# Kernel tuning notes

Measured on AMD Instinct MI355X. Metric: run time of the kernel, lower is better.

## Reference

```python
import jax, jax.numpy as jnp
import numpy as np

EPS = 1e-5

def _ln(x, w, b):
    m = jnp.mean(x, -1, keepdims=True)
    v = jnp.mean((x - m) ** 2, -1, keepdims=True)
    return (x - m) * jax.lax.rsqrt(v + EPS) * w + b

def _silu(x):
    return x * jax.nn.sigmoid(x)

def _mamba(x, in_proj_w, conv_w, conv_b, x_proj_w, dt_proj_w, dt_proj_b, A_log, D, out_proj_w):
    # x: [Bc, L, d_model]; standard mamba_ssm Mamba block math
    Bc, L, _ = x.shape
    d_inner = conv_b.shape[0]
    d_state = A_log.shape[1]
    dt_rank = dt_proj_w.shape[0]
    xz = x @ in_proj_w                          # [Bc, L, 2*d_inner]
    xm, z = jnp.split(xz, 2, axis=-1)
    # causal depthwise conv1d (pad left d_conv-1, truncate to L)
    xm_t = jnp.transpose(xm, (0, 2, 1))         # [Bc, d_inner, L]
    xm_t = jax.lax.conv_general_dilated(
        xm_t, conv_w[:, None, :], (1,), [(conv_w.shape[-1] - 1, 0)],
        dimension_numbers=('NCH', 'OIH', 'NCH'), feature_group_count=d_inner)
    xm = _silu(jnp.transpose(xm_t, (0, 2, 1)) + conv_b)   # [Bc, L, d_inner]
    x_dbl = xm @ x_proj_w                        # [Bc, L, dt_rank + 2*d_state]
    dt_r = x_dbl[..., :dt_rank]
    Bm = x_dbl[..., dt_rank:dt_rank + d_state]
    Cm = x_dbl[..., dt_rank + d_state:]
    dt = jax.nn.softplus(dt_r @ dt_proj_w + dt_proj_b)    # [Bc, L, d_inner]
    A = -jnp.exp(A_log)                          # [d_inner, d_state]

    def step(h, inp):
        xt, dtt, Bt, Ct = inp                    # [Bc,d_inner],[Bc,d_inner],[Bc,d_state],[Bc,d_state]
        dA = jnp.exp(dtt[:, :, None] * A)
        h = dA * h + (dtt * xt)[:, :, None] * Bt[:, None, :]
        y = jnp.einsum('bds,bs->bd', h, Ct)
        return h, y

    h0 = jnp.zeros((Bc, d_inner, d_state), x.dtype)
    xs = (jnp.transpose(xm, (1, 0, 2)), jnp.transpose(dt, (1, 0, 2)),
          jnp.transpose(Bm, (1, 0, 2)), jnp.transpose(Cm, (1, 0, 2)))
    _, ys = jax.lax.scan(step, h0, xs)
    y = jnp.transpose(ys, (1, 0, 2)) + xm * D    # [Bc, L, d_inner]
    y = y * _silu(z)
    return y @ out_proj_w                        # [Bc, L, d_model]

def _pvmamba(x, ln_w, ln_b, skip_scale, proj_w, proj_b, mp):
    # x: [B, H, W, C]; 4 channel-chunks share one Mamba -> batch them as lanes
    B, H, W, C = x.shape
    n = H * W
    d = C // 4
    xf = x.reshape(B, n, C)
    xn = _ln(xf, ln_w, ln_b)
    xc = jnp.transpose(xn.reshape(B, n, 4, d), (2, 0, 1, 3)).reshape(4 * B, n, d)
    ym = _mamba(xc, *mp) + skip_scale * xc
    ym = jnp.transpose(ym.reshape(4, B, n, d), (1, 2, 0, 3)).reshape(B, n, C)
    ym = _ln(ym, ln_w, ln_b)                     # second LN reuses same params (as in source)
    out = ym @ proj_w + proj_b
    return out.reshape(B, H, W, -1)

def _down(x, w):
    # Conv2d k=2 s=2 no bias, exact non-overlapping patch contraction; w: [O, I, 2, 2]
    B, H, W, C = x.shape
    xr = jnp.transpose(x, (0, 3, 1, 2)).reshape(B, C, H // 2, 2, W // 2, 2)
    y = jnp.einsum('bcipjq,ocpq->boij', xr, w)
    return jnp.transpose(y, (0, 2, 3, 1))

def _up(x, w):
    # ConvTranspose2d k=2 s=2 no bias; w: [I, O, 2, 2] (torch layout)
    B, H, W, C = x.shape
    xc = jnp.transpose(x, (0, 3, 1, 2))
    y = jnp.einsum('bcij,copq->boipjq', xc, w).reshape(B, w.shape[1], 2 * H, 2 * W)
    return jnp.transpose(y, (0, 2, 3, 1))

def _mpma(x, ln_w, ln_b, skip_scale, proj_w, proj_b, in_proj_w, conv_w, conv_b,
          x_proj_w, dt_proj_w, dt_proj_b, A_log, D, out_proj_w, down_w, up_w):
    mp = (in_proj_w, conv_w, conv_b, x_proj_w, dt_proj_w, dt_proj_b, A_log, D, out_proj_w)
    xh = jnp.transpose(x, (0, 2, 3, 1))          # NCHW -> NHWC
    outs = [_pvmamba(xh, ln_w, ln_b, skip_scale, proj_w, proj_b, mp)]
    xin = xh
    for _ in range(1, 5):
        xin = _down(xin, down_w)
        outs.append(_pvmamba(xin, ln_w, ln_b, skip_scale, proj_w, proj_b, mp))
    res = outs[-1]
    for l, od in enumerate(outs[-2::-1]):
        res = od + (1.0 / (l + 1)) * _up(res, up_w)
    return jnp.transpose(res, (0, 3, 2, 1))      # note: (0,3,2,1) as in source -> [B,C,W,H]

def setup_inputs() -> dict:
    B, C, HW = 8, 64, 128
    d_model, d_inner, d_state, d_conv, dt_rank = 16, 32, 16, 4, 1
    key = jax.random.key(0)
    ks = jax.random.split(key, 10)
    x = jax.random.normal(ks[0], (B, C, HW, HW), jnp.float32)
    return {
        'x': x,
        'ln_w': jnp.ones((C,), jnp.float32),
        'ln_b': jnp.zeros((C,), jnp.float32),
        'skip_scale': jnp.ones((1,), jnp.float32),
        'proj_w': jax.random.normal(ks[1], (C, C), jnp.float32) * 0.05,
        'proj_b': jnp.zeros((C,), jnp.float32),
        'in_proj_w': jax.random.normal(ks[2], (d_model, 2 * d_inner), jnp.float32) * 0.1,
        'conv_w': jax.random.normal(ks[3], (d_inner, d_conv), jnp.float32) * 0.2,
        'conv_b': jnp.zeros((d_inner,), jnp.float32),
        'x_proj_w': jax.random.normal(ks[4], (d_inner, dt_rank + 2 * d_state), jnp.float32) * 0.1,
        'dt_proj_w': jax.random.normal(ks[5], (dt_rank, d_inner), jnp.float32) * 0.5,
        'dt_proj_b': jnp.full((d_inner,), -4.0, jnp.float32),
        'A_log': jnp.broadcast_to(jnp.log(jnp.arange(1, d_state + 1, dtype=jnp.float32)), (d_inner, d_state)),
        'D': jnp.ones((d_inner,), jnp.float32),
        'out_proj_w': jax.random.normal(ks[6], (d_inner, d_model), jnp.float32) * 0.1,
        'down_w': jax.random.normal(ks[7], (C, C, 2, 2), jnp.float32) * 0.05,
        'up_w': jax.random.normal(ks[8], (C, C, 2, 2), jnp.float32) * 0.05,
    }

def reference(x, ln_w, ln_b, skip_scale, proj_w, proj_b, in_proj_w, conv_w, conv_b,
              x_proj_w, dt_proj_w, dt_proj_b, A_log, D, out_proj_w, down_w, up_w):
    return _mpma(x, ln_w, ln_b, skip_scale, proj_w, proj_b, in_proj_w, conv_w, conv_b,
                 x_proj_w, dt_proj_w, dt_proj_b, A_log, D, out_proj_w, down_w, up_w)
```

## Files before the change

kernel.cpp:

```cpp
#include <hip/hip_runtime.h>

#define TMAX 128

__device__ __forceinline__ float silu_f(float x) {
    return x / (1.f + __expf(-x));
}
__device__ __forceinline__ float softplus_f(float x) {
    return (x > 20.f) ? x : log1pf(__expf(x));
}

__global__ __launch_bounds__(256) void k_tr_in(const float* __restrict__ x, float* __restrict__ xh) {
    __shared__ float tile[128 * 65];
    int h = blockIdx.x, b = blockIdx.y;
    const float* ip = x + (size_t)b * 64 * 16384 + (size_t)h * 128;
    for (int i = threadIdx.x; i < 64 * 128; i += 256) {
        int c = i >> 7, w = i & 127;
        tile[w * 65 + c] = ip[(size_t)c * 16384 + w];
    }
    __syncthreads();
    float* op = xh + ((size_t)(b * 128 + h)) * 128 * 64;
    for (int i = threadIdx.x; i < 128 * 64; i += 256) {
        int w = i >> 6, c = i & 63;
        op[i] = tile[w * 65 + c];
    }
}

__global__ __launch_bounds__(256) void k_tr_out(const float* __restrict__ res, float* __restrict__ out) {
    __shared__ float tile[64 * 129];
    int w = blockIdx.x, b = blockIdx.y;
    const float* ip = res + (size_t)b * 16384 * 64 + (size_t)w * 64;
    for (int i = threadIdx.x; i < 128 * 64; i += 256) {
        int h = i >> 6, c = i & 63;
        tile[c * 129 + h] = ip[(size_t)h * 128 * 64 + c];
    }
    __syncthreads();
    float* op = out + (size_t)b * 64 * 16384 + (size_t)w * 128;
    for (int i = threadIdx.x; i < 64 * 128; i += 256) {
        int c = i >> 7, hh = i & 127;
        op[(size_t)c * 16384 + hh] = tile[c * 129 + hh];
    }
}

__global__ __launch_bounds__(256) void k_down(const float* __restrict__ in, float* __restrict__ out,
                                              const float* __restrict__ dwp, int Ho, int Wo, int ntot) {
    __shared__ float dw[16384];
    for (int i = threadIdx.x; i < 16384; i += 256) {
        int o = i & 63, cpq = i >> 6;
        dw[cpq * 64 + o] = dwp[o * 256 + cpq];
    }
    __syncthreads();
    int gid = blockIdx.x * 256 + threadIdx.x;
    if (gid >= ntot) return;
    int og = gid & 3, pix = gid >> 2;
    int j = pix % Wo, i2 = (pix / Wo) % Ho, b = pix / (Wo * Ho);
    const float* ip = in + (((size_t)b * (2 * Ho) + 2 * i2) * (size_t)(2 * Wo) + 2 * j) * 64;
    float acc[16];
#pragma unroll
    for (int m = 0; m < 16; ++m) acc[m] = 0.f;
    for (int p = 0; p < 2; ++p) {
        for (int q = 0; q < 2; ++q) {
            const float* xp = ip + ((size_t)p * (2 * Wo) + q) * 64;
            for (int c = 0; c < 64; ++c) {
                float xv = xp[c];
                const float* wrow = &dw[(c * 4 + p * 2 + q) * 64 + og * 16];
#pragma unroll
                for (int m = 0; m < 16; ++m) acc[m] = fmaf(xv, wrow[m], acc[m]);
            }
        }
    }
    float* op = out + (size_t)pix * 64 + og * 16;
#pragma unroll
    for (int m = 0; m < 4; ++m) {
        float4 v = make_float4(acc[m * 4], acc[m * 4 + 1], acc[m * 4 + 2], acc[m * 4 + 3]);
        *(float4*)(op + m * 4) = v;
    }
}

__global__ __launch_bounds__(256) void k_up(const float* __restrict__ src, float* __restrict__ dst,
                                            const float* __restrict__ uwp, int H, int W, float coef, int ntot) {
    __shared__ float uw[16384];
    for (int i = threadIdx.x; i < 16384; i += 256) {
        int o = i & 63, cpq = i >> 6;
        int c = cpq >> 2, pq = cpq & 3;
        uw[cpq * 64 + o] = uwp[c * 256 + o * 4 + pq];
    }
    __syncthreads();
    int gid = blockIdx.x * 256 + threadIdx.x;
    if (gid >= ntot) return;
    int og = gid & 3, pix = gid >> 2;
    int x = pix % W, y = (pix / W) % H, b = pix / (W * H);
    int Hs = H >> 1, Ws = W >> 1;
    int pq = (y & 1) * 2 + (x & 1);
    const float* sp = src + (((size_t)b * Hs + (y >> 1)) * (size_t)Ws + (x >> 1)) * 64;
    float acc[16];
#pragma unroll
    for (int m = 0; m < 16; ++m) acc[m] = 0.f;
    for (int c = 0; c < 64; ++c) {
        float xv = sp[c];
        const float* wrow = &uw[(c * 4 + pq) * 64 + og * 16];
#pragma unroll
        for (int m = 0; m < 16; ++m) acc[m] = fmaf(xv, wrow[m], acc[m]);
    }
    float* op = dst + (size_t)pix * 64 + og * 16;
#pragma unroll
    for (int m = 0; m < 4; ++m) {
        float4 cur = *(float4*)(op + m * 4);
        cur.x += coef * acc[m * 4];
        cur.y += coef * acc[m * 4 + 1];
        cur.z += coef * acc[m * 4 + 2];
        cur.w += coef * acc[m * 4 + 3];
        *(float4*)(op + m * 4) = cur;
    }
}

__global__ __launch_bounds__(256) void k_ln(const float* __restrict__ in, float* __restrict__ out,
                                            const float* __restrict__ w, const float* __restrict__ bb, int ntok) {
    int t = blockIdx.x * 256 + threadIdx.x;
    if (t >= ntok) return;
    const float4* p = (const float4*)(in + (size_t)t * 64);
    float4 v[16];
    float s = 0.f;
#pragma unroll
    for (int i = 0; i < 16; ++i) {
        v[i] = p[i];
        s += v[i].x + v[i].y + v[i].z + v[i].w;
    }
    float m = s * (1.f / 64.f);
    float q = 0.f;
#pragma unroll
    for (int i = 0; i < 16; ++i) {
        float a = v[i].x - m, b2 = v[i].y - m, c = v[i].z - m, d = v[i].w - m;
        q += a * a + b2 * b2 + c * c + d * d;
    }
    float r = rsqrtf(q * (1.f / 64.f) + 1e-5f);
    float4* o = (float4*)(out + (size_t)t * 64);
    const float4* w4 = (const float4*)w;
    const float4* b4 = (const float4*)bb;
#pragma unroll
    for (int i = 0; i < 16; ++i) {
        float4 ww = w4[i], bbv = b4[i];
        float4 ov;
        ov.x = (v[i].x - m) * r * ww.x + bbv.x;
        ov.y = (v[i].y - m) * r * ww.y + bbv.y;
        ov.z = (v[i].z - m) * r * ww.z + bbv.z;
        ov.w = (v[i].w - m) * r * ww.w + bbv.w;
        o[i] = ov;
    }
}

__global__ __launch_bounds__(256) void k_post(const float* __restrict__ ym, float* __restrict__ outl,
                                              const float* __restrict__ lnw, const float* __restrict__ lnb,
                                              const float* __restrict__ proj_w, const float* __restrict__ proj_b,
                                              int ntok) {
    __shared__ float pw[4096];
    __shared__ float pb[64];
    __shared__ float lw[64], lb[64];
    for (int i = threadIdx.x; i < 4096; i += 256) pw[i] = proj_w[i];
    if (threadIdx.x < 64) {
        pb[threadIdx.x] = proj_b[threadIdx.x];
        lw[threadIdx.x] = lnw[threadIdx.x];
        lb[threadIdx.x] = lnb[threadIdx.x];
    }
    __syncthreads();
    int t = blockIdx.x * 256 + threadIdx.x;
    if (t >= ntok) return;
    const float4* p = (const float4*)(ym + (size_t)t * 64);
    float4 v[16];
    float s = 0.f;
#pragma unroll
    for (int i = 0; i < 16; ++i) {
        v[i] = p[i];
        s += v[i].x + v[i].y + v[i].z + v[i].w;
    }
    float m = s * (1.f / 64.f);
    float q = 0.f;
#pragma unroll
    for (int i = 0; i < 16; ++i) {
        float a = v[i].x - m, b2 = v[i].y - m, c = v[i].z - m, d = v[i].w - m;
        q += a * a + b2 * b2 + c * c + d * d;
    }
    float r = rsqrtf(q * (1.f / 64.f) + 1e-5f);
    float* op = outl + (size_t)t * 64;
    for (int half = 0; half < 2; ++half) {
        float acc[32];
#pragma unroll
        for (int o = 0; o < 32; ++o) acc[o] = pb[half * 32 + o];
#pragma unroll
        for (int i = 0; i < 16; ++i) {
            float vals[4] = {v[i].x, v[i].y, v[i].z, v[i].w};
#pragma unroll
            for (int k = 0; k < 4; ++k) {
                int c = i * 4 + k;
                float vn = (vals[k] - m) * r * lw[c] + lb[c];
                const float* wrow = &pw[c * 64 + half * 32];
#pragma unroll
                for (int o = 0; o < 32; ++o) acc[o] = fmaf(vn, wrow[o], acc[o]);
            }
        }
#pragma unroll
        for (int mq = 0; mq < 8; ++mq) {
            float4 ov = make_float4(acc[mq * 4], acc[mq * 4 + 1], acc[mq * 4 + 2], acc[mq * 4 + 3]);
            *(float4*)(op + half * 32 + mq * 4) = ov;
        }
    }
}

template <int PHASE>
__global__ __launch_bounds__(256, 2) void k_scan(const float* __restrict__ xn,
                                                 float* __restrict__ Pbuf, float* __restrict__ Hbuf,
                                                 const float* __restrict__ hinbuf, float* __restrict__ ym,
                                                 const float* __restrict__ in_proj_w, const float* __restrict__ conv_w,
                                                 const float* __restrict__ conv_b, const float* __restrict__ x_proj_w,
                                                 const float* __restrict__ dt_w, const float* __restrict__ dt_b,
                                                 const float* __restrict__ A_log, const float* __restrict__ Dvec,
                                                 const float* __restrict__ out_proj_w, const float* __restrict__ skip_scale,
                                                 int n, int nch) {
    __shared__ float Wm[16][32];
    __shared__ float Wz[16][32];
    __shared__ float cw[32][4];
    __shared__ float cb[32];
    __shared__ float Wxp[32][33];
    __shared__ float dtw[32], dtb[32];
    __shared__ float Ash[32][16];
    __shared__ float Dsh[32];
    __shared__ float Wout[32][16];
    __shared__ float xmpre_y[(TMAX + 3) * 32];
    __shared__ float dt_s[TMAX][32];
    __shared__ float xm_s[TMAX][32];
    __shared__ float Bs[TMAX][16];
    __shared__ float Cs[TMAX][16];

    const int tid = threadIdx.x;
    const int chunk = blockIdx.x;
    const int seq = blockIdx.y;
    const int g = seq >> 3, b = seq & 7;
    const int t0 = chunk * TMAX;
    const int Tc = (n - t0 < TMAX) ? (n - t0) : TMAX;

    for (int i = tid; i < 16 * 32; i += 256) {
        int k = i >> 5, d = i & 31;
        Wm[k][d] = in_proj_w[k * 64 + d];
        Wz[k][d] = in_proj_w[k * 64 + 32 + d];
    }
    for (int i = tid; i < 32 * 4; i += 256) cw[i >> 2][i & 3] = conv_w[i];
    if (tid < 32) {
        cb[tid] = conv_b[tid];
        dtw[tid] = dt_w[tid];
        dtb[tid] = dt_b[tid];
        Dsh[tid] = Dvec[tid];
    }
    for (int i = tid; i < 32 * 33; i += 256) Wxp[i / 33][i % 33] = x_proj_w[i];
    for (int i = tid; i < 32 * 16; i += 256) {
        Ash[i >> 4][i & 15] = -__expf(A_log[i]);
        Wout[i >> 4][i & 15] = out_proj_w[i];
    }
    __syncthreads();

    const float* xbase = xn + (size_t)b * n * 64 + g * 16;

    if (tid < Tc + 3) {
        int t = t0 + tid - 3;
        float* dst = &xmpre_y[tid * 32];
        if (t < 0) {
#pragma unroll
            for (int d = 0; d < 32; ++d) dst[d] = 0.f;
        } else {
            const float4* xp = (const float4*)(xbase + (size_t)t * 64);
            float4 x0 = xp[0], x1 = xp[1], x2 = xp[2], x3 = xp[3];
            float xc[16] = {x0.x, x0.y, x0.z, x0.w, x1.x, x1.y, x1.z, x1.w,
                            x2.x, x2.y, x2.z, x2.w, x3.x, x3.y, x3.z, x3.w};
#pragma unroll
            for (int d = 0; d < 32; ++d) {
                float a = 0.f;
#pragma unroll
                for (int k = 0; k < 16; ++k) a = fmaf(xc[k], Wm[k][d], a);
                dst[d] = a;
            }
        }
    }
    __syncthreads();

    if (tid < Tc) {
        float xmv[32];
#pragma unroll
        for (int d = 0; d < 32; ++d) {
            float a = cb[d];
#pragma unroll
            for (int k = 0; k < 4; ++k) a = fmaf(xmpre_y[(tid + k) * 32 + d], cw[d][k], a);
            float sv = silu_f(a);
            xmv[d] = sv;
            xm_s[tid][d] = sv;
        }
        float dtr = 0.f;
#pragma unroll
        for (int d = 0; d < 32; ++d) dtr = fmaf(xmv[d], Wxp[d][0], dtr);
#pragma unroll
        for (int s = 0; s < 16; ++s) {
            float bv = 0.f;
#pragma unroll
            for (int d = 0; d < 32; ++d) bv = fmaf(xmv[d], Wxp[d][1 + s], bv);
            Bs[tid][s] = bv;
            if (PHASE == 1) {
                float cv = 0.f;
#pragma unroll
                for (int d = 0; d < 32; ++d) cv = fmaf(xmv[d], Wxp[d][17 + s], cv);
                Cs[tid][s] = cv;
            }
        }
#pragma unroll
        for (int d = 0; d < 32; ++d) dt_s[tid][d] = softplus_f(fmaf(dtr, dtw[d], dtb[d]));
    }
    __syncthreads();

    const int d = tid >> 3;
    const int s0 = (tid & 7) * 2;
    const float a0 = Ash[d][s0], a1 = Ash[d][s0 + 1];
    float h0, h1;
    const size_t cbi = ((size_t)seq * nch + chunk) * 512 + tid * 2;
    if (PHASE == 1) {
        float2 hi = *(const float2*)&hinbuf[cbi];
        h0 = hi.x;
        h1 = hi.y;
    } else {
        h0 = 0.f;
        h1 = 0.f;
    }
    float sdt = 0.f;
#pragma unroll 2
    for (int t = 0; t < Tc; ++t) {
        float dtv = dt_s[t][d];
        float u = dtv * xm_s[t][d];
        float2 bb2 = *(const float2*)&Bs[t][s0];
        float e0 = __expf(dtv * a0), e1 = __expf(dtv * a1);
        h0 = fmaf(e0, h0, u * bb2.x);
        h1 = fmaf(e1, h1, u * bb2.y);
        if (PHASE == 0) {
            sdt += dtv;
        } else {
            float2 cc = *(const float2*)&Cs[t][s0];
            float pp = fmaf(h0, cc.x, h1 * cc.y);
            pp += __shfl_xor(pp, 1);
            pp += __shfl_xor(pp, 2);
            pp += __shfl_xor(pp, 4);
            if ((tid & 7) == 0) xmpre_y[t * 32 + d] = pp;
        }
    }
    if (PHASE == 0) {
        float2 pv;
        pv.x = __expf(a0 * sdt);
        pv.y = __expf(a1 * sdt);
        *(float2*)&Pbuf[cbi] = pv;
        float2 hv;
        hv.x = h0;
        hv.y = h1;
        *(float2*)&Hbuf[cbi] = hv;
    } else {
        __syncthreads();
        if (tid < Tc) {
            int t = t0 + tid;
            const float4* xp = (const float4*)(xbase + (size_t)t * 64);
            float4 x0 = xp[0], x1 = xp[1], x2 = xp[2], x3 = xp[3];
            float xc[16] = {x0.x, x0.y, x0.z, x0.w, x1.x, x1.y, x1.z, x1.w,
                            x2.x, x2.y, x2.z, x2.w, x3.x, x3.y, x3.z, x3.w};
            float yv[32];
#pragma unroll
            for (int dd = 0; dd < 32; ++dd) {
                float zz = 0.f;
#pragma unroll
                for (int k = 0; k < 16; ++k) zz = fmaf(xc[k], Wz[k][dd], zz);
                float yb = xmpre_y[tid * 32 + dd] + xm_s[tid][dd] * Dsh[dd];
                yv[dd] = yb * silu_f(zz);
            }
            float ss = skip_scale[0];
            float* ymtok = ym + ((size_t)b * n + t) * 64 + g * 16;
#pragma unroll
            for (int jq = 0; jq < 4; ++jq) {
                float4 ov;
                float o0 = 0.f, o1 = 0.f, o2 = 0.f, o3 = 0.f;
#pragma unroll
                for (int dd = 0; dd < 32; ++dd) {
                    o0 = fmaf(yv[dd], Wout[dd][jq * 4 + 0], o0);
                    o1 = fmaf(yv[dd], Wout[dd][jq * 4 + 1], o1);
                    o2 = fmaf(yv[dd], Wout[dd][jq * 4 + 2], o2);
                    o3 = fmaf(yv[dd], Wout[dd][jq * 4 + 3], o3);
                }
                ov.x = o0 + ss * xc[jq * 4 + 0];
                ov.y = o1 + ss * xc[jq * 4 + 1];
                ov.z = o2 + ss * xc[jq * 4 + 2];
                ov.w = o3 + ss * xc[jq * 4 + 3];
                *(float4*)(ymtok + jq * 4) = ov;
            }
        }
    }
}

__global__ __launch_bounds__(256) void k_scanB(const float* __restrict__ P, const float* __restrict__ Hl,
                                               float* __restrict__ hin, int nch) {
    int idx = blockIdx.x * 256 + threadIdx.x;
    int seq = idx >> 9, ds = idx & 511;
    size_t base = (size_t)seq * nch * 512 + ds;
    float h = 0.f;
    for (int k = 0; k < nch; ++k) {
        hin[base + (size_t)k * 512] = h;
        h = fmaf(P[base + (size_t)k * 512], h, Hl[base + (size_t)k * 512]);
    }
}

extern "C" void kernel_launch(void* const* d_in, const int* in_sizes, int n_in,
                              void* d_out, int out_size, void* d_ws, size_t ws_size,
                              hipStream_t stream) {
    (void)in_sizes; (void)n_in; (void)out_size; (void)ws_size;
    const float* x          = (const float*)d_in[0];
    const float* ln_w       = (const float*)d_in[1];
    const float* ln_b       = (const float*)d_in[2];
    const float* skip_scale = (const float*)d_in[3];
    const float* proj_w     = (const float*)d_in[4];
    const float* proj_b     = (const float*)d_in[5];
    const float* in_proj_w  = (const float*)d_in[6];
    const float* conv_w     = (const float*)d_in[7];
    const float* conv_b     = (const float*)d_in[8];
    const float* x_proj_w   = (const float*)d_in[9];
    const float* dt_proj_w  = (const float*)d_in[10];
    const float* dt_proj_b  = (const float*)d_in[11];
    const float* A_log      = (const float*)d_in[12];
    const float* Dv         = (const float*)d_in[13];
    const float* out_proj_w = (const float*)d_in[14];
    const float* down_w     = (const float*)d_in[15];
    const float* up_w       = (const float*)d_in[16];
    float* out = (float*)d_out;
    float* ws = (float*)d_ws;

    static const int nl[5] = {16384, 4096, 1024, 256, 64};
    static const size_t off_xh[5] = {0, 8388608, 10485760, 11010048, 11141120};
    static const size_t off_out[5] = {11173888, 19562496, 21659648, 22183936, 22315008};
    const size_t off_xn = 22347776;
    const size_t off_P = 30736384;
    const size_t off_H = 32833536;
    const size_t off_hin = 34930688;
    const size_t off_ym = 0;

    k_tr_in<<<dim3(128, 8), dim3(256), 0, stream>>>(x, ws + off_xh[0]);

    for (int l = 0; l < 4; ++l) {
        int Ho = 128 >> (l + 1);
        int ntot = 8 * Ho * Ho * 4;
        k_down<<<dim3((ntot + 255) / 256), dim3(256), 0, stream>>>(ws + off_xh[l], ws + off_xh[l + 1],
                                                                   down_w, Ho, Ho, ntot);
    }

    for (int l = 0; l < 5; ++l) {
        int n = nl[l];
        int ntok = 8 * n;
        int nch = (n + TMAX - 1) / TMAX;
        k_ln<<<dim3((ntok + 255) / 256), dim3(256), 0, stream>>>(ws + off_xh[l], ws + off_xn, ln_w, ln_b, ntok);
        k_scan<0><<<dim3(nch, 32), dim3(256), 0, stream>>>(ws + off_xn, ws + off_P, ws + off_H, nullptr, nullptr,
                                                           in_proj_w, conv_w, conv_b, x_proj_w, dt_proj_w, dt_proj_b,
                                                           A_log, Dv, out_proj_w, skip_scale, n, nch);
        k_scanB<<<dim3(64), dim3(256), 0, stream>>>(ws + off_P, ws + off_H, ws + off_hin, nch);
        k_scan<1><<<dim3(nch, 32), dim3(256), 0, stream>>>(ws + off_xn, nullptr, nullptr, ws + off_hin, ws + off_ym,
                                                           in_proj_w, conv_w, conv_b, x_proj_w, dt_proj_w, dt_proj_b,
                                                           A_log, Dv, out_proj_w, skip_scale, n, nch);
        k_post<<<dim3((ntok + 255) / 256), dim3(256), 0, stream>>>(ws + off_ym, ws + off_out[l], ln_w, ln_b,
                                                                   proj_w, proj_b, ntok);
    }

    static const float coefs[4] = {1.f, 0.5f, 1.f / 3.f, 0.25f};
    for (int k = 0; k < 4; ++k) {
        int l = 3 - k;
        int H = 128 >> l;
        int ntot = 8 * H * H * 4;
        k_up<<<dim3((ntot + 255) / 256), dim3(256), 0, stream>>>(ws + off_out[l + 1], ws + off_out[l],
                                                                 up_w, H, H, coefs[k], ntot);
    }

    k_tr_out<<<dim3(128, 8), dim3(256), 0, stream>>>(ws + off_out[0], out);
}
```

Before: 1.636 ms.

## Precompute scan inputs once into fp16 stream; split chunked scan into pre/A/B/C kernels

LayerNorm, in_proj, conv, x_proj and dt projection now run once in a k_pre kernel. It writes dt, x, B and C as half2 into a time-contiguous stream buffer, replacing the old two-phase scan that recomputed these projections in both phases. The scan kernels then read compact fp16 data directly from global memory, and the final phase fuses LN recomputation, gating and out_proj. The trade-offs are fp16 rounding of scan inputs, per-step global loads with no shared staging, and extra launches when the workspace forces the sequences to be split.

```diff
diff --git a/kernel.cpp b/kernel.cpp
--- a/kernel.cpp
+++ b/kernel.cpp
@@ -1,4 +1,5 @@
 #include <hip/hip_runtime.h>
+#include <hip/hip_fp16.h>
 
 #define TMAX 128
 
@@ -113,38 +114,256 @@
     }
 }
 
-__global__ __launch_bounds__(256) void k_ln(const float* __restrict__ in, float* __restrict__ out,
-                                            const float* __restrict__ w, const float* __restrict__ bb, int ntok) {
-    int t = blockIdx.x * 256 + threadIdx.x;
-    if (t >= ntok) return;
-    const float4* p = (const float4*)(in + (size_t)t * 64);
-    float4 v[16];
-    float s = 0.f;
-#pragma unroll
-    for (int i = 0; i < 16; ++i) {
-        v[i] = p[i];
-        s += v[i].x + v[i].y + v[i].z + v[i].w;
-    }
-    float m = s * (1.f / 64.f);
-    float q = 0.f;
-#pragma unroll
-    for (int i = 0; i < 16; ++i) {
-        float a = v[i].x - m, b2 = v[i].y - m, c = v[i].z - m, d = v[i].w - m;
-        q += a * a + b2 * b2 + c * c + d * d;
-    }
-    float r = rsqrtf(q * (1.f / 64.f) + 1e-5f);
-    float4* o = (float4*)(out + (size_t)t * 64);
-    const float4* w4 = (const float4*)w;
-    const float4* b4 = (const float4*)bb;
-#pragma unroll
-    for (int i = 0; i < 16; ++i) {
-        float4 ww = w4[i], bbv = b4[i];
-        float4 ov;
-        ov.x = (v[i].x - m) * r * ww.x + bbv.x;
-        ov.y = (v[i].y - m) * r * ww.y + bbv.y;
-        ov.z = (v[i].z - m) * r * ww.z + bbv.z;
-        ov.w = (v[i].w - m) * r * ww.w + bbv.w;
-        o[i] = ov;
+__global__ __launch_bounds__(256) void k_pre(const float* __restrict__ xh, __half2* __restrict__ stream,
+                                             const float* __restrict__ lnw, const float* __restrict__ lnb,
+                                             const float* __restrict__ in_proj_w, const float* __restrict__ conv_w,
+                                             const float* __restrict__ conv_b, const float* __restrict__ x_proj_w,
+                                             const float* __restrict__ dt_w, const float* __restrict__ dt_b,
+                                             int n, int nseq, int seq_base) {
+    __shared__ float pre[259][33];
+    __shared__ float Wm[16][32];
+    __shared__ float Wxp[32][33];
+    __shared__ float cw[32][4];
+    __shared__ float cb[32], dtw[32], dtb[32];
+    __shared__ float lw[64], lb[64];
+    const int tid = threadIdx.x;
+    const int t0 = blockIdx.x * 256;
+    const int seqL = blockIdx.y;
+    const int seqG = seq_base + seqL;
+    const int b = seqG >> 2, g = seqG & 3;
+
+    for (int i = tid; i < 512; i += 256) Wm[i >> 5][i & 31] = in_proj_w[(i >> 5) * 64 + (i & 31)];
+    for (int i = tid; i < 32 * 33; i += 256) Wxp[i / 33][i % 33] = x_proj_w[i];
+    for (int i = tid; i < 128; i += 256) cw[i >> 2][i & 3] = conv_w[i];
+    if (tid < 32) { cb[tid] = conv_b[tid]; dtw[tid] = dt_w[tid]; dtb[tid] = dt_b[tid]; }
+    if (tid < 64) { lw[tid] = lnw[tid]; lb[tid] = lnb[tid]; }
+    __syncthreads();
+
+    const int Tcb = min(256, n - t0);
+    const int rows = Tcb + 3;
+    for (int r = tid; r < rows; r += 256) {
+        int t = t0 + r - 3;
+        if (t < 0) {
+#pragma unroll
+            for (int d = 0; d < 32; ++d) pre[r][d] = 0.f;
+        } else {
+            const float4* xp = (const float4*)(xh + ((size_t)b * n + t) * 64);
+            float4 v[16];
+            float s = 0.f;
+#pragma unroll
+            for (int i = 0; i < 16; ++i) { v[i] = xp[i]; s += v[i].x + v[i].y + v[i].z + v[i].w; }
+            float m = s * (1.f / 64.f);
+            float q = 0.f;
+#pragma unroll
+            for (int i = 0; i < 16; ++i) {
+                float a = v[i].x - m, b2 = v[i].y - m, c = v[i].z - m, dd = v[i].w - m;
+                q += a * a + b2 * b2 + c * c + dd * dd;
+            }
+            float rr = rsqrtf(q * (1.f / 64.f) + 1e-5f);
+            const float4* xg = (const float4*)(xh + ((size_t)b * n + t) * 64 + g * 16);
+            float xn16[16];
+#pragma unroll
+            for (int i = 0; i < 4; ++i) {
+                float4 u4 = xg[i];
+                int c0 = g * 16 + i * 4;
+                xn16[i * 4 + 0] = (u4.x - m) * rr * lw[c0 + 0] + lb[c0 + 0];
+                xn16[i * 4 + 1] = (u4.y - m) * rr * lw[c0 + 1] + lb[c0 + 1];
+                xn16[i * 4 + 2] = (u4.z - m) * rr * lw[c0 + 2] + lb[c0 + 2];
+                xn16[i * 4 + 3] = (u4.w - m) * rr * lw[c0 + 3] + lb[c0 + 3];
+            }
+#pragma unroll
+            for (int d = 0; d < 32; ++d) {
+                float a = 0.f;
+#pragma unroll
+                for (int j = 0; j < 16; ++j) a = fmaf(xn16[j], Wm[j][d], a);
+                pre[r][d] = a;
+            }
+        }
+    }
+    __syncthreads();
+
+    if (tid < Tcb) {
+        const int t = t0 + tid;
+        float xmv[32];
+#pragma unroll
+        for (int d = 0; d < 32; ++d) {
+            float a = cb[d];
+#pragma unroll
+            for (int k = 0; k < 4; ++k) a = fmaf(pre[tid + k][d], cw[d][k], a);
+            xmv[d] = silu_f(a);
+        }
+        float dtr = 0.f;
+#pragma unroll
+        for (int d = 0; d < 32; ++d) dtr = fmaf(xmv[d], Wxp[d][0], dtr);
+        const size_t sb = (size_t)seqL * n + t;
+#pragma unroll
+        for (int d = 0; d < 32; ++d) {
+            float dtv = softplus_f(fmaf(dtr, dtw[d], dtb[d]));
+            stream[(size_t)d * nseq * n + sb] = __floats2half2_rn(dtv, xmv[d]);
+        }
+#pragma unroll
+        for (int p = 0; p < 8; ++p) {
+            float b0 = 0.f, b1 = 0.f;
+#pragma unroll
+            for (int d = 0; d < 32; ++d) {
+                b0 = fmaf(xmv[d], Wxp[d][1 + 2 * p], b0);
+                b1 = fmaf(xmv[d], Wxp[d][2 + 2 * p], b1);
+            }
+            stream[(size_t)(32 + p) * nseq * n + sb] = __floats2half2_rn(b0, b1);
+        }
+#pragma unroll
+        for (int p = 0; p < 8; ++p) {
+            float c0 = 0.f, c1 = 0.f;
+#pragma unroll
+            for (int d = 0; d < 32; ++d) {
+                c0 = fmaf(xmv[d], Wxp[d][17 + 2 * p], c0);
+                c1 = fmaf(xmv[d], Wxp[d][18 + 2 * p], c1);
+            }
+            stream[(size_t)(40 + p) * nseq * n + sb] = __floats2half2_rn(c0, c1);
+        }
+    }
+}
+
+__global__ __launch_bounds__(256) void k_scanA(const __half2* __restrict__ stream, float* __restrict__ P,
+                                               float* __restrict__ H, const float* __restrict__ A_log,
+                                               int n, int nseq, int nch) {
+    const int tid = threadIdx.x;
+    const int d = tid >> 3, ss = tid & 7;
+    const int chunk = blockIdx.x, seqL = blockIdx.y;
+    const int t0 = chunk * TMAX;
+    const int Tc = min(TMAX, n - t0);
+    const float a0 = -__expf(A_log[d * 16 + 2 * ss]);
+    const float a1 = -__expf(A_log[d * 16 + 2 * ss + 1]);
+    const __half2* pdx = stream + ((size_t)d * nseq + seqL) * n + t0;
+    const __half2* pB = stream + ((size_t)(32 + ss) * nseq + seqL) * n + t0;
+    float h0 = 0.f, h1 = 0.f, sdt = 0.f;
+    for (int t = 0; t < Tc; ++t) {
+        float2 dx = __half22float2(pdx[t]);
+        float2 bv = __half22float2(pB[t]);
+        float u = dx.x * dx.y;
+        h0 = fmaf(__expf(a0 * dx.x), h0, u * bv.x);
+        h1 = fmaf(__expf(a1 * dx.x), h1, u * bv.y);
+        sdt += dx.x;
+    }
+    const size_t cbi = ((size_t)seqL * nch + chunk) * 512 + tid * 2;
+    *(float2*)&P[cbi] = make_float2(__expf(a0 * sdt), __expf(a1 * sdt));
+    *(float2*)&H[cbi] = make_float2(h0, h1);
+}
+
+__global__ __launch_bounds__(256) void k_scanB(const float* __restrict__ P, const float* __restrict__ Hl,
+                                               float* __restrict__ hin, int nch, int nseq) {
+    int idx = blockIdx.x * 256 + threadIdx.x;
+    if (idx >= nseq * 512) return;
+    int seq = idx >> 9, ds = idx & 511;
+    size_t base = (size_t)seq * nch * 512 + ds;
+    float h = 0.f;
+    for (int k = 0; k < nch; ++k) {
+        hin[base + (size_t)k * 512] = h;
+        h = fmaf(P[base + (size_t)k * 512], h, Hl[base + (size_t)k * 512]);
+    }
+}
+
+__global__ __launch_bounds__(256) void k_scanC(const __half2* __restrict__ stream, const float* __restrict__ hin,
+                                               const float* __restrict__ xh, float* __restrict__ ym,
+                                               const float* __restrict__ A_log,
+                                               const float* __restrict__ lnw, const float* __restrict__ lnb,
+                                               const float* __restrict__ in_proj_w, const float* __restrict__ Dvec,
+                                               const float* __restrict__ out_proj_w,
+                                               const float* __restrict__ skip_scale,
+                                               int n, int nseq, int seq_base, int nch) {
+    __shared__ float yb[TMAX][33];
+    __shared__ float Wz[16][32];
+    __shared__ float Wout[32][16];
+    __shared__ float lw[64], lb[64];
+    __shared__ float Dsh[32];
+    const int tid = threadIdx.x;
+    const int d = tid >> 3, ss = tid & 7;
+    const int chunk = blockIdx.x, seqL = blockIdx.y;
+    const int seqG = seq_base + seqL;
+    const int b = seqG >> 2, g = seqG & 3;
+    const int t0 = chunk * TMAX;
+    const int Tc = min(TMAX, n - t0);
+
+    for (int i = tid; i < 512; i += 256) Wz[i >> 5][i & 31] = in_proj_w[(i >> 5) * 64 + 32 + (i & 31)];
+    for (int i = tid; i < 512; i += 256) Wout[i >> 4][i & 15] = out_proj_w[i];
+    if (tid < 64) { lw[tid] = lnw[tid]; lb[tid] = lnb[tid]; }
+    if (tid < 32) Dsh[tid] = Dvec[tid];
+
+    const float a0 = -__expf(A_log[d * 16 + 2 * ss]);
+    const float a1 = -__expf(A_log[d * 16 + 2 * ss + 1]);
+    const __half2* pdx = stream + ((size_t)d * nseq + seqL) * n + t0;
+    const __half2* pB = stream + ((size_t)(32 + ss) * nseq + seqL) * n + t0;
+    const __half2* pC = stream + ((size_t)(40 + ss) * nseq + seqL) * n + t0;
+    const size_t cbi = ((size_t)seqL * nch + chunk) * 512 + tid * 2;
+    float2 hi2 = *(const float2*)&hin[cbi];
+    float h0 = hi2.x, h1 = hi2.y;
+
+    for (int t = 0; t < Tc; ++t) {
+        float2 dx = __half22float2(pdx[t]);
+        float2 bv = __half22float2(pB[t]);
+        float2 cv = __half22float2(pC[t]);
+        float u = dx.x * dx.y;
+        h0 = fmaf(__expf(a0 * dx.x), h0, u * bv.x);
+        h1 = fmaf(__expf(a1 * dx.x), h1, u * bv.y);
+        float pp = fmaf(h0, cv.x, h1 * cv.y);
+        pp += __shfl_xor(pp, 1);
+        pp += __shfl_xor(pp, 2);
+        pp += __shfl_xor(pp, 4);
+        if (ss == 0) yb[t][d] = pp;
+    }
+    __syncthreads();
+
+    if (tid < Tc) {
+        const int t = t0 + tid;
+        const float4* xp = (const float4*)(xh + ((size_t)b * n + t) * 64);
+        float4 v[16];
+        float s = 0.f;
+#pragma unroll
+        for (int i = 0; i < 16; ++i) { v[i] = xp[i]; s += v[i].x + v[i].y + v[i].z + v[i].w; }
+        float m = s * (1.f / 64.f);
+        float q = 0.f;
+#pragma unroll
+        for (int i = 0; i < 16; ++i) {
+            float a = v[i].x - m, b2 = v[i].y - m, c = v[i].z - m, dd = v[i].w - m;
+            q += a * a + b2 * b2 + c * c + dd * dd;
+        }
+        float rr = rsqrtf(q * (1.f / 64.f) + 1e-5f);
+        const float4* xg = (const float4*)(xh + ((size_t)b * n + t) * 64 + g * 16);
+        float xc[16];
+#pragma unroll
+        for (int i = 0; i < 4; ++i) {
+            float4 u4 = xg[i];
+            int c0 = g * 16 + i * 4;
+            xc[i * 4 + 0] = (u4.x - m) * rr * lw[c0 + 0] + lb[c0 + 0];
+            xc[i * 4 + 1] = (u4.y - m) * rr * lw[c0 + 1] + lb[c0 + 1];
+            xc[i * 4 + 2] = (u4.z - m) * rr * lw[c0 + 2] + lb[c0 + 2];
+            xc[i * 4 + 3] = (u4.w - m) * rr * lw[c0 + 3] + lb[c0 + 3];
+        }
+        float yv[32];
+#pragma unroll
+        for (int dd = 0; dd < 32; ++dd) {
+            float2 dx = __half22float2(stream[((size_t)dd * nseq + seqL) * n + t0 + tid]);
+            float zz = 0.f;
+#pragma unroll
+            for (int j = 0; j < 16; ++j) zz = fmaf(xc[j], Wz[j][dd], zz);
+            yv[dd] = (yb[tid][dd] + dx.y * Dsh[dd]) * silu_f(zz);
+        }
+        float sscale = skip_scale[0];
+        float* ymtok = ym + ((size_t)b * n + t) * 64 + g * 16;
+#pragma unroll
+        for (int jq = 0; jq < 4; ++jq) {
+            float o0 = 0.f, o1 = 0.f, o2 = 0.f, o3 = 0.f;
+#pragma unroll
+            for (int dd = 0; dd < 32; ++dd) {
+                o0 = fmaf(yv[dd], Wout[dd][jq * 4 + 0], o0);
+                o1 = fmaf(yv[dd], Wout[dd][jq * 4 + 1], o1);
+                o2 = fmaf(yv[dd], Wout[dd][jq * 4 + 2], o2);
+                o3 = fmaf(yv[dd], Wout[dd][jq * 4 + 3], o3);
+            }
+            float4 ov = make_float4(o0 + sscale * xc[jq * 4 + 0], o1 + sscale * xc[jq * 4 + 1],
+                                    o2 + sscale * xc[jq * 4 + 2], o3 + sscale * xc[jq * 4 + 3]);
+            *(float4*)(ymtok + jq * 4) = ov;
+        }
     }
 }
 
@@ -205,211 +424,10 @@
     }
 }
 
-template <int PHASE>
-__global__ __launch_bounds__(256, 2) void k_scan(const float* __restrict__ xn,
-                                                 float* __restrict__ Pbuf, float* __restrict__ Hbuf,
-                                                 const float* __restrict__ hinbuf, float* __restrict__ ym,
-                                                 const float* __restrict__ in_proj_w, const float* __restrict__ conv_w,
-                                                 const float* __restrict__ conv_b, const float* __restrict__ x_proj_w,
-                                                 const float* __restrict__ dt_w, const float* __restrict__ dt_b,
-                                                 const float* __restrict__ A_log, const float* __restrict__ Dvec,
-                                                 const float* __restrict__ out_proj_w, const float* __restrict__ skip_scale,
-                                                 int n, int nch) {
-    __shared__ float Wm[16][32];
-    __shared__ float Wz[16][32];
-    __shared__ float cw[32][4];
-    __shared__ float cb[32];
-    __shared__ float Wxp[32][33];
-    __shared__ float dtw[32], dtb[32];
-    __shared__ float Ash[32][16];
-    __shared__ float Dsh[32];
-    __shared__ float Wout[32][16];
-    __shared__ float xmpre_y[(TMAX + 3) * 32];
-    __shared__ float dt_s[TMAX][32];
-    __shared__ float xm_s[TMAX][32];
-    __shared__ float Bs[TMAX][16];
-    __shared__ float Cs[TMAX][16];
-
-    const int tid = threadIdx.x;
-    const int chunk = blockIdx.x;
-    const int seq = blockIdx.y;
-    const int g = seq >> 3, b = seq & 7;
-    const int t0 = chunk * TMAX;
-    const int Tc = (n - t0 < TMAX) ? (n - t0) : TMAX;
-
-    for (int i = tid; i < 16 * 32; i += 256) {
-        int k = i >> 5, d = i & 31;
-        Wm[k][d] = in_proj_w[k * 64 + d];
-        Wz[k][d] = in_proj_w[k * 64 + 32 + d];
-    }
-    for (int i = tid; i < 32 * 4; i += 256) cw[i >> 2][i & 3] = conv_w[i];
-    if (tid < 32) {
-        cb[tid] = conv_b[tid];
-        dtw[tid] = dt_w[tid];
-        dtb[tid] = dt_b[tid];
-        Dsh[tid] = Dvec[tid];
-    }
-    for (int i = tid; i < 32 * 33; i += 256) Wxp[i / 33][i % 33] = x_proj_w[i];
-    for (int i = tid; i < 32 * 16; i += 256) {
-        Ash[i >> 4][i & 15] = -__expf(A_log[i]);
-        Wout[i >> 4][i & 15] = out_proj_w[i];
-    }
-    __syncthreads();
-
-    const float* xbase = xn + (size_t)b * n * 64 + g * 16;
-
-    if (tid < Tc + 3) {
-        int t = t0 + tid - 3;
-        float* dst = &xmpre_y[tid * 32];
-        if (t < 0) {
-#pragma unroll
-            for (int d = 0; d < 32; ++d) dst[d] = 0.f;
-        } else {
-            const float4* xp = (const float4*)(xbase + (size_t)t * 64);
-            float4 x0 = xp[0], x1 = xp[1], x2 = xp[2], x3 = xp[3];
-            float xc[16] = {x0.x, x0.y, x0.z, x0.w, x1.x, x1.y, x1.z, x1.w,
-                            x2.x, x2.y, x2.z, x2.w, x3.x, x3.y, x3.z, x3.w};
-#pragma unroll
-            for (int d = 0; d < 32; ++d) {
-                float a = 0.f;
-#pragma unroll
-                for (int k = 0; k < 16; ++k) a = fmaf(xc[k], Wm[k][d], a);
-                dst[d] = a;
-            }
-        }
-    }
-    __syncthreads();
-
-    if (tid < Tc) {
-        float xmv[32];
-#pragma unroll
-        for (int d = 0; d < 32; ++d) {
-            float a = cb[d];
-#pragma unroll
-            for (int k = 0; k < 4; ++k) a = fmaf(xmpre_y[(tid + k) * 32 + d], cw[d][k], a);
-            float sv = silu_f(a);
-            xmv[d] = sv;
-            xm_s[tid][d] = sv;
-        }
-        float dtr = 0.f;
-#pragma unroll
-        for (int d = 0; d < 32; ++d) dtr = fmaf(xmv[d], Wxp[d][0], dtr);
-#pragma unroll
-        for (int s = 0; s < 16; ++s) {
-            float bv = 0.f;
-#pragma unroll
-            for (int d = 0; d < 32; ++d) bv = fmaf(xmv[d], Wxp[d][1 + s], bv);
-            Bs[tid][s] = bv;
-            if (PHASE == 1) {
-                float cv = 0.f;
-#pragma unroll
-                for (int d = 0; d < 32; ++d) cv = fmaf(xmv[d], Wxp[d][17 + s], cv);
-                Cs[tid][s] = cv;
-            }
-        }
-#pragma unroll
-        for (int d = 0; d < 32; ++d) dt_s[tid][d] = softplus_f(fmaf(dtr, dtw[d], dtb[d]));
-    }
-    __syncthreads();
-
-    const int d = tid >> 3;
-    const int s0 = (tid & 7) * 2;
-    const float a0 = Ash[d][s0], a1 = Ash[d][s0 + 1];
-    float h0, h1;
-    const size_t cbi = ((size_t)seq * nch + chunk) * 512 + tid * 2;
-    if (PHASE == 1) {
-        float2 hi = *(const float2*)&hinbuf[cbi];
-        h0 = hi.x;
-        h1 = hi.y;
-    } else {
-        h0 = 0.f;
-        h1 = 0.f;
-    }
-    float sdt = 0.f;
-#pragma unroll 2
-    for (int t = 0; t < Tc; ++t) {
-        float dtv = dt_s[t][d];
-        float u = dtv * xm_s[t][d];
-        float2 bb2 = *(const float2*)&Bs[t][s0];
-        float e0 = __expf(dtv * a0), e1 = __expf(dtv * a1);
-        h0 = fmaf(e0, h0, u * bb2.x);
-        h1 = fmaf(e1, h1, u * bb2.y);
-        if (PHASE == 0) {
-            sdt += dtv;
-        } else {
-            float2 cc = *(const float2*)&Cs[t][s0];
-            float pp = fmaf(h0, cc.x, h1 * cc.y);
-            pp += __shfl_xor(pp, 1);
-            pp += __shfl_xor(pp, 2);
-            pp += __shfl_xor(pp, 4);
-            if ((tid & 7) == 0) xmpre_y[t * 32 + d] = pp;
-        }
-    }
-    if (PHASE == 0) {
-        float2 pv;
-        pv.x = __expf(a0 * sdt);
-        pv.y = __expf(a1 * sdt);
-        *(float2*)&Pbuf[cbi] = pv;
-        float2 hv;
-        hv.x = h0;
-        hv.y = h1;
-        *(float2*)&Hbuf[cbi] = hv;
-    } else {
-        __syncthreads();
-        if (tid < Tc) {
-            int t = t0 + tid;
-            const float4* xp = (const float4*)(xbase + (size_t)t * 64);
-            float4 x0 = xp[0], x1 = xp[1], x2 = xp[2], x3 = xp[3];
-            float xc[16] = {x0.x, x0.y, x0.z, x0.w, x1.x, x1.y, x1.z, x1.w,
-                            x2.x, x2.y, x2.z, x2.w, x3.x, x3.y, x3.z, x3.w};
-            float yv[32];
-#pragma unroll
-            for (int dd = 0; dd < 32; ++dd) {
-                float zz = 0.f;
-#pragma unroll
-                for (int k = 0; k < 16; ++k) zz = fmaf(xc[k], Wz[k][dd], zz);
-                float yb = xmpre_y[tid * 32 + dd] + xm_s[tid][dd] * Dsh[dd];
-                yv[dd] = yb * silu_f(zz);
-            }
-            float ss = skip_scale[0];
-            float* ymtok = ym + ((size_t)b * n + t) * 64 + g * 16;
-#pragma unroll
-            for (int jq = 0; jq < 4; ++jq) {
-                float4 ov;
-                float o0 = 0.f, o1 = 0.f, o2 = 0.f, o3 = 0.f;
-#pragma unroll
-                for (int dd = 0; dd < 32; ++dd) {
-                    o0 = fmaf(yv[dd], Wout[dd][jq * 4 + 0], o0);
-                    o1 = fmaf(yv[dd], Wout[dd][jq * 4 + 1], o1);
-                    o2 = fmaf(yv[dd], Wout[dd][jq * 4 + 2], o2);
-                    o3 = fmaf(yv[dd], Wout[dd][jq * 4 + 3], o3);
-                }
-                ov.x = o0 + ss * xc[jq * 4 + 0];
-                ov.y = o1 + ss * xc[jq * 4 + 1];
-                ov.z = o2 + ss * xc[jq * 4 + 2];
-                ov.w = o3 + ss * xc[jq * 4 + 3];
-                *(float4*)(ymtok + jq * 4) = ov;
-            }
-        }
-    }
-}
-
-__global__ __launch_bounds__(256) void k_scanB(const float* __restrict__ P, const float* __restrict__ Hl,
-                                               float* __restrict__ hin, int nch) {
-    int idx = blockIdx.x * 256 + threadIdx.x;
-    int seq = idx >> 9, ds = idx & 511;
-    size_t base = (size_t)seq * nch * 512 + ds;
-    float h = 0.f;
-    for (int k = 0; k < nch; ++k) {
-        hin[base + (size_t)k * 512] = h;
-        h = fmaf(P[base + (size_t)k * 512], h, Hl[base + (size_t)k * 512]);
-    }
-}
-
 extern "C" void kernel_launch(void* const* d_in, const int* in_sizes, int n_in,
                               void* d_out, int out_size, void* d_ws, size_t ws_size,
-                              hipStream_t stream) {
-    (void)in_sizes; (void)n_in; (void)out_size; (void)ws_size;
+                              hipStream_t stream_) {
+    (void)in_sizes; (void)n_in; (void)out_size;
     const float* x          = (const float*)d_in[0];
     const float* ln_w       = (const float*)d_in[1];
     const float* ln_b       = (const float*)d_in[2];
@@ -432,36 +450,42 @@
 
     static const int nl[5] = {16384, 4096, 1024, 256, 64};
     static const size_t off_xh[5] = {0, 8388608, 10485760, 11010048, 11141120};
-    static const size_t off_out[5] = {11173888, 19562496, 21659648, 22183936, 22315008};
-    const size_t off_xn = 22347776;
-    const size_t off_P = 30736384;
-    const size_t off_H = 32833536;
-    const size_t off_hin = 34930688;
-    const size_t off_ym = 0;
-
-    k_tr_in<<<dim3(128, 8), dim3(256), 0, stream>>>(x, ws + off_xh[0]);
+    const size_t OFF_YM = 11173888;
+    static const size_t off_out[5] = {19562496, 27951104, 30048256, 30572544, 30703616};
+    const size_t OFF_P = 30736384, OFF_H = 32833536, OFF_HIN = 34930688;
+    const size_t STR_BYTE_OFF = 37027840ULL * 4ULL;
+    __half2* strm = (__half2*)((char*)d_ws + STR_BYTE_OFF);
+
+    k_tr_in<<<dim3(128, 8), dim3(256), 0, stream_>>>(x, ws + off_xh[0]);
 
     for (int l = 0; l < 4; ++l) {
         int Ho = 128 >> (l + 1);
         int ntot = 8 * Ho * Ho * 4;
-        k_down<<<dim3((ntot + 255) / 256), dim3(256), 0, stream>>>(ws + off_xh[l], ws + off_xh[l + 1],
-                                                                   down_w, Ho, Ho, ntot);
+        k_down<<<dim3((ntot + 255) / 256), dim3(256), 0, stream_>>>(ws + off_xh[l], ws + off_xh[l + 1],
+                                                                    down_w, Ho, Ho, ntot);
     }
 
     for (int l = 0; l < 5; ++l) {
         int n = nl[l];
         int ntok = 8 * n;
         int nch = (n + TMAX - 1) / TMAX;
-        k_ln<<<dim3((ntok + 255) / 256), dim3(256), 0, stream>>>(ws + off_xh[l], ws + off_xn, ln_w, ln_b, ntok);
-        k_scan<0><<<dim3(nch, 32), dim3(256), 0, stream>>>(ws + off_xn, ws + off_P, ws + off_H, nullptr, nullptr,
-                                                           in_proj_w, conv_w, conv_b, x_proj_w, dt_proj_w, dt_proj_b,
-                                                           A_log, Dv, out_proj_w, skip_scale, n, nch);
-        k_scanB<<<dim3(64), dim3(256), 0, stream>>>(ws + off_P, ws + off_H, ws + off_hin, nch);
-        k_scan<1><<<dim3(nch, 32), dim3(256), 0, stream>>>(ws + off_xn, nullptr, nullptr, ws + off_hin, ws + off_ym,
-                                                           in_proj_w, conv_w, conv_b, x_proj_w, dt_proj_w, dt_proj_b,
-                                                           A_log, Dv, out_proj_w, skip_scale, n, nch);
-        k_post<<<dim3((ntok + 255) / 256), dim3(256), 0, stream>>>(ws + off_ym, ws + off_out[l], ln_w, ln_b,
-                                                                   proj_w, proj_b, ntok);
+        int nblk = (n + 255) / 256;
+        int Sl = 1;
+        while (Sl < 32 && STR_BYTE_OFF + (size_t)192 * (32 / Sl) * n > ws_size) Sl <<= 1;
+        int nseq = 32 / Sl;
+        for (int sp = 0; sp < Sl; ++sp) {
+            int sb = sp * nseq;
+            k_pre<<<dim3(nblk, nseq), dim3(256), 0, stream_>>>(ws + off_xh[l], strm, ln_w, ln_b, in_proj_w,
+                                                               conv_w, conv_b, x_proj_w, dt_proj_w, dt_proj_b,
+                                                               n, nseq, sb);
+            k_scanA<<<dim3(nch, nseq), dim3(256), 0, stream_>>>(strm, ws + OFF_P, ws + OFF_H, A_log, n, nseq, nch);
+            k_scanB<<<dim3(nseq * 2), dim3(256), 0, stream_>>>(ws + OFF_P, ws + OFF_H, ws + OFF_HIN, nch, nseq);
+            k_scanC<<<dim3(nch, nseq), dim3(256), 0, stream_>>>(strm, ws + OFF_HIN, ws + off_xh[l], ws + OFF_YM,
+                                                                A_log, ln_w, ln_b, in_proj_w, Dv, out_proj_w,
+                                                                skip_scale, n, nseq, sb, nch);
+        }
+        k_post<<<dim3((ntok + 255) / 256), dim3(256), 0, stream_>>>(ws + OFF_YM, ws + off_out[l], ln_w, ln_b,
+                                                                    proj_w, proj_b, ntok);
     }
 
     static const float coefs[4] = {1.f, 0.5f, 1.f / 3.f, 0.25f};
@@ -469,9 +493,9 @@
         int l = 3 - k;
         int H = 128 >> l;
         int ntot = 8 * H * H * 4;
-        k_up<<<dim3((ntot + 255) / 256), dim3(256), 0, stream>>>(ws + off_out[l + 1], ws + off_out[l],
-                                                                 up_w, H, H, coefs[k], ntot);
-    }
-
-    k_tr_out<<<dim3(128, 8), dim3(256), 0, stream>>>(ws + off_out[0], out);
-}
+        k_up<<<dim3((ntot + 255) / 256), dim3(256), 0, stream_>>>(ws + off_out[l + 1], ws + off_out[l],
+                                                                  up_w, H, H, coefs[k], ntot);
+    }
+
+    k_tr_out<<<dim3(128, 8), dim3(256), 0, stream_>>>(ws + off_out[0], out);
+}
```

New measurement: 1.654 ms. No clear change (+1.1%).
